# Optimization experiments

Measured on AMD Instinct MI355X. Metric: run time of the kernel, lower is better.

Reference implementation:

```python
import jax, jax.numpy as jnp
import numpy as np

B = 8388608  # batch

def moth(x, a, b):
    # per-feature parametric elementwise activation: a * x * sigmoid(b * x)
    return a * x * jax.nn.sigmoid(b * x)

def setup_inputs() -> dict:
    key = jax.random.key(0)
    ks = jax.random.split(key, 12)
    inp = {
        'x':  jax.random.normal(ks[0], (B, 2), dtype=jnp.float32),
        'W1': jax.random.normal(ks[1], (2, 8), dtype=jnp.float32) * (1.0 / np.sqrt(2)),
        'b1': jax.random.normal(ks[2], (8,), dtype=jnp.float32) * 0.01,
        'a1': jax.random.normal(ks[3], (8,), dtype=jnp.float32) * 0.1 + 1.0,
        'c1': jax.random.normal(ks[4], (8,), dtype=jnp.float32) * 0.1 + 1.0,
        'W2': jax.random.normal(ks[5], (8, 4), dtype=jnp.float32) * (1.0 / np.sqrt(8)),
        'b2': jax.random.normal(ks[6], (4,), dtype=jnp.float32) * 0.01,
        'a2': jax.random.normal(ks[7], (4,), dtype=jnp.float32) * 0.1 + 1.0,
        'c2': jax.random.normal(ks[8], (4,), dtype=jnp.float32) * 0.1 + 1.0,
        'W3': jax.random.normal(ks[9], (4, 1), dtype=jnp.float32) * (1.0 / np.sqrt(4)),
        'b3': jax.random.normal(ks[10], (1,), dtype=jnp.float32) * 0.01,
    }
    return inp

def reference(x, W1, b1, a1, c1, W2, b2, a2, c2, W3, b3):
    h = x @ W1 + b1            # [B, 8]
    h = moth(h, a1, c1)        # [B, 8]
    h = h @ W2 + b2            # [B, 4]
    h = moth(h, a2, c2)        # [B, 4]
    out = h @ W3 + b3          # [B, 1]
    return out
```

## Files before the change

kernel.cpp:

```cpp
#include <hip/hip_runtime.h>

#define NLOG2E -1.44269504088896340736f


__global__ __launch_bounds__(256, 2) void PlaygroundModel_66365834658304_kernel(
    const float* __restrict__ x,
    const float* __restrict__ W1, const float* __restrict__ b1,
    const float* __restrict__ a1, const float* __restrict__ c1,
    const float* __restrict__ W2, const float* __restrict__ b2,
    const float* __restrict__ a2, const float* __restrict__ c2,
    const float* __restrict__ W3, const float* __restrict__ b3,
    float* __restrict__ out, int rows)
{
    int tid = blockIdx.x * blockDim.x + threadIdx.x;
    long long base = (long long)tid * 4;
    if (base >= rows) return;

    float w1a[8], w1b[8], bb1[8], ncl1[8];
#pragma unroll
    for (int j = 0; j < 8; ++j) {
        w1a[j]  = W1[j];
        w1b[j]  = W1[8 + j];
        bb1[j]  = b1[j];
        ncl1[j] = c1[j] * NLOG2E;
    }
    float w2f[32];
#pragma unroll
    for (int j = 0; j < 8; ++j) {
        float a = a1[j];
#pragma unroll
        for (int k = 0; k < 4; ++k) w2f[j * 4 + k] = a * W2[j * 4 + k];
    }
    float bb2[4], ncl2[4], aw[4];
#pragma unroll
    for (int k = 0; k < 4; ++k) {
        bb2[k]  = b2[k];
        ncl2[k] = c2[k] * NLOG2E;
        aw[k]   = a2[k] * W3[k];
    }
    float bb3 = b3[0];

    if (base + 3 < rows) {
        const float4* x4 = (const float4*)x;
        float4 p0 = x4[(size_t)tid * 2 + 0];
        float4 p1 = x4[(size_t)tid * 2 + 1];
        float xs0[4] = {p0.x, p0.z, p1.x, p1.z};
        float xs1[4] = {p0.y, p0.w, p1.y, p1.w};
        float r[4];
#pragma unroll
        for (int r4 = 0; r4 < 4; ++r4) {
            float x0 = xs0[r4], x1 = xs1[r4];
            float h[8];
#pragma unroll
            for (int j = 0; j < 8; ++j) {
                float t = fmaf(x0, w1a[j], fmaf(x1, w1b[j], bb1[j]));
                float s = __builtin_amdgcn_rcpf(
                              1.0f + __builtin_amdgcn_exp2f(ncl1[j] * t));
                h[j] = t * s;
            }
            float o = bb3;
#pragma unroll
            for (int k = 0; k < 4; ++k) {
                float t = bb2[k];
#pragma unroll
                for (int j = 0; j < 8; ++j) t = fmaf(h[j], w2f[j * 4 + k], t);
                float s = __builtin_amdgcn_rcpf(
                              1.0f + __builtin_amdgcn_exp2f(ncl2[k] * t));
                o = fmaf(t * s, aw[k], o);
            }
            r[r4] = o;
        }
        float4 ov = make_float4(r[0], r[1], r[2], r[3]);
        ((float4*)out)[tid] = ov;
    } else {
        for (long long rr = base; rr < rows; ++rr) {
            float x0 = x[rr * 2 + 0], x1 = x[rr * 2 + 1];
            float h[8];
#pragma unroll
            for (int j = 0; j < 8; ++j) {
                float t = fmaf(x0, w1a[j], fmaf(x1, w1b[j], bb1[j]));
                float s = __builtin_amdgcn_rcpf(
                              1.0f + __builtin_amdgcn_exp2f(ncl1[j] * t));
                h[j] = t * s;
            }
            float o = bb3;
#pragma unroll
            for (int k = 0; k < 4; ++k) {
                float t = bb2[k];
#pragma unroll
                for (int j = 0; j < 8; ++j) t = fmaf(h[j], w2f[j * 4 + k], t);
                float s = __builtin_amdgcn_rcpf(
                              1.0f + __builtin_amdgcn_exp2f(ncl2[k] * t));
                o = fmaf(t * s, aw[k], o);
            }
            out[rr] = o;
        }
    }
}

extern "C" void kernel_launch(void* const* d_in, const int* in_sizes, int n_in,
                              void* d_out, int out_size, void* d_ws, size_t ws_size,
                              hipStream_t stream) {
    const float* x  = (const float*)d_in[0];
    const float* W1 = (const float*)d_in[1];
    const float* b1 = (const float*)d_in[2];
    const float* a1 = (const float*)d_in[3];
    const float* c1 = (const float*)d_in[4];
    const float* W2 = (const float*)d_in[5];
    const float* b2 = (const float*)d_in[6];
    const float* a2 = (const float*)d_in[7];
    const float* c2 = (const float*)d_in[8];
    const float* W3 = (const float*)d_in[9];
    const float* b3 = (const float*)d_in[10];
    float* out = (float*)d_out;

    int rows  = in_sizes[0] / 2;
    int rows4 = (rows + 3) / 4;
    int block = 256;
    int grid  = (rows4 + block - 1) / block;

    PlaygroundModel_66365834658304_kernel<<<grid, block, 0, stream>>>(
        x, W1, b1, a1, c1, W2, b2, a2, c2, W3, b3, out, rows);
}
```

Baseline: 128.5 us.

## Process eight rows per thread and stop pre-folding weight constants into registers

Each thread now handles eight rows with four float4 loads and two float4 stores, which halves the grid. The weights are read directly inside a force-inlined per-row helper instead of being folded into register arrays. The a1 and a2 scales are applied per row rather than folded into W2 and W3, so each row does extra multiplies. Launch bounds rise to four blocks per SM to push occupancy higher, which risks spills or more per-row arithmetic.

```diff
diff --git a/kernel.cpp b/kernel.cpp
--- a/kernel.cpp
+++ b/kernel.cpp
@@ -3,7 +3,36 @@
 #define NLOG2E -1.44269504088896340736f
 
 
-__global__ __launch_bounds__(256, 2) void PlaygroundModel_66365834658304_kernel(
+__device__ __forceinline__ float swish_row(
+    float x0, float x1,
+    const float* __restrict__ W1, const float* __restrict__ b1,
+    const float* __restrict__ a1, const float* ncl1,
+    const float* __restrict__ W2, const float* __restrict__ b2,
+    const float* __restrict__ a2, const float* ncl2,
+    const float* __restrict__ W3, float bb3)
+{
+    float h[8];
+#pragma unroll
+    for (int j = 0; j < 8; ++j) {
+        float t = fmaf(x0, W1[j], fmaf(x1, W1[8 + j], b1[j]));
+        float s = __builtin_amdgcn_rcpf(
+                      1.0f + __builtin_amdgcn_exp2f(ncl1[j] * t));
+        h[j] = a1[j] * (t * s);
+    }
+    float o = bb3;
+#pragma unroll
+    for (int k = 0; k < 4; ++k) {
+        float t = b2[k];
+#pragma unroll
+        for (int j = 0; j < 8; ++j) t = fmaf(h[j], W2[j * 4 + k], t);
+        float s = __builtin_amdgcn_rcpf(
+                      1.0f + __builtin_amdgcn_exp2f(ncl2[k] * t));
+        o = fmaf(a2[k] * (t * s), W3[k], o);
+    }
+    return o;
+}
+
+__global__ __launch_bounds__(256, 4) void PlaygroundModel_66365834658304_kernel(
     const float* __restrict__ x,
     const float* __restrict__ W1, const float* __restrict__ b1,
     const float* __restrict__ a1, const float* __restrict__ c1,
@@ -13,87 +42,37 @@
     float* __restrict__ out, int rows)
 {
     int tid = blockIdx.x * blockDim.x + threadIdx.x;
-    long long base = (long long)tid * 4;
+    long long base = (long long)tid * 8;
     if (base >= rows) return;
 
-    float w1a[8], w1b[8], bb1[8], ncl1[8];
+    float ncl1[8], ncl2[4];
 #pragma unroll
-    for (int j = 0; j < 8; ++j) {
-        w1a[j]  = W1[j];
-        w1b[j]  = W1[8 + j];
-        bb1[j]  = b1[j];
-        ncl1[j] = c1[j] * NLOG2E;
-    }
-    float w2f[32];
+    for (int j = 0; j < 8; ++j) ncl1[j] = c1[j] * NLOG2E;
 #pragma unroll
-    for (int j = 0; j < 8; ++j) {
-        float a = a1[j];
-#pragma unroll
-        for (int k = 0; k < 4; ++k) w2f[j * 4 + k] = a * W2[j * 4 + k];
-    }
-    float bb2[4], ncl2[4], aw[4];
-#pragma unroll
-    for (int k = 0; k < 4; ++k) {
-        bb2[k]  = b2[k];
-        ncl2[k] = c2[k] * NLOG2E;
-        aw[k]   = a2[k] * W3[k];
-    }
+    for (int k = 0; k < 4; ++k) ncl2[k] = c2[k] * NLOG2E;
     float bb3 = b3[0];
 
-    if (base + 3 < rows) {
+    if (base + 7 < rows) {
         const float4* x4 = (const float4*)x;
-        float4 p0 = x4[(size_t)tid * 2 + 0];
-        float4 p1 = x4[(size_t)tid * 2 + 1];
-        float xs0[4] = {p0.x, p0.z, p1.x, p1.z};
-        float xs1[4] = {p0.y, p0.w, p1.y, p1.w};
-        float r[4];
+        float4 p0 = x4[(size_t)tid * 4 + 0];
+        float4 p1 = x4[(size_t)tid * 4 + 1];
+        float4 p2 = x4[(size_t)tid * 4 + 2];
+        float4 p3 = x4[(size_t)tid * 4 + 3];
+        float X0[8] = {p0.x, p0.z, p1.x, p1.z, p2.x, p2.z, p3.x, p3.z};
+        float X1[8] = {p0.y, p0.w, p1.y, p1.w, p2.y, p2.w, p3.y, p3.w};
+        float r[8];
 #pragma unroll
-        for (int r4 = 0; r4 < 4; ++r4) {
-            float x0 = xs0[r4], x1 = xs1[r4];
-            float h[8];
-#pragma unroll
-            for (int j = 0; j < 8; ++j) {
-                float t = fmaf(x0, w1a[j], fmaf(x1, w1b[j], bb1[j]));
-                float s = __builtin_amdgcn_rcpf(
-                              1.0f + __builtin_amdgcn_exp2f(ncl1[j] * t));
-                h[j] = t * s;
-            }
-            float o = bb3;
-#pragma unroll
-            for (int k = 0; k < 4; ++k) {
-                float t = bb2[k];
-#pragma unroll
-                for (int j = 0; j < 8; ++j) t = fmaf(h[j], w2f[j * 4 + k], t);
-                float s = __builtin_amdgcn_rcpf(
-                              1.0f + __builtin_amdgcn_exp2f(ncl2[k] * t));
-                o = fmaf(t * s, aw[k], o);
-            }
-            r[r4] = o;
-        }
-        float4 ov = make_float4(r[0], r[1], r[2], r[3]);
-        ((float4*)out)[tid] = ov;
+        for (int rr = 0; rr < 8; ++rr)
+            r[rr] = swish_row(X0[rr], X1[rr], W1, b1, a1, ncl1,
+                              W2, b2, a2, ncl2, W3, bb3);
+        float4* o4 = (float4*)out;
+        o4[(size_t)tid * 2 + 0] = make_float4(r[0], r[1], r[2], r[3]);
+        o4[(size_t)tid * 2 + 1] = make_float4(r[4], r[5], r[6], r[7]);
     } else {
         for (long long rr = base; rr < rows; ++rr) {
             float x0 = x[rr * 2 + 0], x1 = x[rr * 2 + 1];
-            float h[8];
-#pragma unroll
-            for (int j = 0; j < 8; ++j) {
-                float t = fmaf(x0, w1a[j], fmaf(x1, w1b[j], bb1[j]));
-                float s = __builtin_amdgcn_rcpf(
-                              1.0f + __builtin_amdgcn_exp2f(ncl1[j] * t));
-                h[j] = t * s;
-            }
-            float o = bb3;
-#pragma unroll
-            for (int k = 0; k < 4; ++k) {
-                float t = bb2[k];
-#pragma unroll
-                for (int j = 0; j < 8; ++j) t = fmaf(h[j], w2f[j * 4 + k], t);
-                float s = __builtin_amdgcn_rcpf(
-                              1.0f + __builtin_amdgcn_exp2f(ncl2[k] * t));
-                o = fmaf(t * s, aw[k], o);
-            }
-            out[rr] = o;
+            out[rr] = swish_row(x0, x1, W1, b1, a1, ncl1,
+                                W2, b2, a2, ncl2, W3, bb3);
         }
     }
 }
@@ -115,9 +94,9 @@
     float* out = (float*)d_out;
 
     int rows  = in_sizes[0] / 2;
-    int rows4 = (rows + 3) / 4;
+    int rows8 = (rows + 7) / 8;
     int block = 256;
-    int grid  = (rows4 + block - 1) / block;
+    int grid  = (rows8 + block - 1) / block;
 
     PlaygroundModel_66365834658304_kernel<<<grid, block, 0, stream>>>(
         x, W1, b1, a1, c1, W2, b2, a2, c2, W3, b3, out, rows);
```

Result: no change. 130.4 us (+1.5%).
